# Kernel optimization log

Measured on AMD Instinct MI355X. Metric: run time of the kernel, lower is better.

## Reference

```python
import jax, jax.numpy as jnp
import numpy as np

SCALING = 32.0 / 16.0  # alpha / rank

def setup_inputs() -> dict:
    key = jax.random.key(0)
    k1, k2, k3, k4, k5 = jax.random.split(key, 5)
    B, S, D_IN, D_OUT, R = 4, 2048, 4096, 4096, 16
    x = jax.random.normal(k1, (B, S, D_IN), dtype=jnp.float32)
    weight_int = jax.random.randint(k2, (D_OUT, D_IN), -128, 128, dtype=jnp.int32)
    weight_scale = jax.random.uniform(k3, (1,), dtype=jnp.float32) * 0.01 + 1e-4
    lora_A = jax.random.normal(k4, (R, D_IN), dtype=jnp.float32) * (1.0 / np.sqrt(D_IN))
    lora_B = jax.random.normal(k5, (D_OUT, R), dtype=jnp.float32) * 0.02
    return {"x": x, "weight_int": weight_int, "weight_scale": weight_scale,
            "lora_A": lora_A, "lora_B": lora_B}

def reference(x, weight_int, weight_scale, lora_A, lora_B):
    # Dequantized base weight: [out, in]
    w = weight_int.astype(jnp.float32) * weight_scale  # broadcast scalar scale
    base = jnp.einsum('bsi,oi->bso', x, w)
    # Low-rank LoRA path: (x @ A^T) @ B^T * scaling
    lora = jnp.einsum('bsr,or->bso', jnp.einsum('bsi,ri->bsr', x, lora_A), lora_B) * SCALING
    return base + lora
```

## Files before the change

kernel.cpp:

```cpp
#include <hip/hip_runtime.h>

constexpr int M = 8192;
constexpr int N = 4096;
constexpr int K = 4096;
constexpr float SCALING = 2.0f;

typedef __bf16 bf16x8 __attribute__((ext_vector_type(8)));
typedef __bf16 bf16x4 __attribute__((ext_vector_type(4)));
typedef float  f32x4  __attribute__((ext_vector_type(4)));

__global__ __launch_bounds__(256) void qlora_cast_x(const float* __restrict__ x,
                                                    __bf16* __restrict__ xb) {
    const size_t i = ((size_t)blockIdx.x * 256 + threadIdx.x) * 8;
    const float4 v0 = *(const float4*)(x + i);
    const float4 v1 = *(const float4*)(x + i + 4);
    bf16x8 o;
    o[0] = (__bf16)v0.x; o[1] = (__bf16)v0.y; o[2] = (__bf16)v0.z; o[3] = (__bf16)v0.w;
    o[4] = (__bf16)v1.x; o[5] = (__bf16)v1.y; o[6] = (__bf16)v1.z; o[7] = (__bf16)v1.w;
    *(bf16x8*)(xb + i) = o;
}

__global__ __launch_bounds__(256) void qlora_prep_w(const int* __restrict__ wi,
                                                    const float* __restrict__ wscale,
                                                    const float* __restrict__ lA,
                                                    const float* __restrict__ lB,
                                                    __bf16* __restrict__ W) {
    __shared__ __align__(16) float As[16][1028];
    const int t  = threadIdx.x;
    const int ol = t >> 4;
    const int kk = t & 15;
    const int o  = blockIdx.x * 16 + ol;
    const float s = wscale[0];
    float b[16];
#pragma unroll
    for (int r = 0; r < 16; ++r) b[r] = lB[o * 16 + r];

    for (int c = 0; c < 4; ++c) {
        const int c0 = c * 1024;
#pragma unroll
        for (int i = 0; i < 16; ++i) {
            const int idx = t + i * 256;
            const int r   = idx >> 8;
            const int c4  = idx & 255;
            const float4 v = *(const float4*)(lA + r * K + c0 + c4 * 4);
            *(float4*)(&As[r][c4 * 4]) = v;
        }
        __syncthreads();
#pragma unroll
        for (int j = 0; j < 16; ++j) {
            const int k4 = kk + j * 16;
            const int kg = c0 + k4 * 4;
            const int4 w4 = *(const int4*)(wi + (size_t)o * K + kg);
            float a0 = 0.f, a1 = 0.f, a2 = 0.f, a3 = 0.f;
#pragma unroll
            for (int r = 0; r < 16; ++r) {
                const float4 a4 = *(const float4*)(&As[r][k4 * 4]);
                a0 += b[r] * a4.x; a1 += b[r] * a4.y;
                a2 += b[r] * a4.z; a3 += b[r] * a4.w;
            }
            bf16x4 v;
            v[0] = (__bf16)((float)w4.x * s + SCALING * a0);
            v[1] = (__bf16)((float)w4.y * s + SCALING * a1);
            v[2] = (__bf16)((float)w4.z * s + SCALING * a2);
            v[3] = (__bf16)((float)w4.w * s + SCALING * a3);
            *(bf16x4*)(W + (size_t)o * K + kg) = v;
        }
        __syncthreads();
    }
}

__device__ __forceinline__ void async16(const __bf16* g, __bf16* l) {
    __builtin_amdgcn_global_load_lds(
        (const __attribute__((address_space(1))) unsigned int*)(unsigned long long)g,
        (__attribute__((address_space(3))) unsigned int*)(unsigned int)(unsigned long long)l,
        16, 0, 0);
}

__global__ __launch_bounds__(512, 2) void qlora_gemm_bt(const __bf16* __restrict__ A,
                                                        const __bf16* __restrict__ B,
                                                        float* __restrict__ C) {
    __shared__ __align__(16) __bf16 Lds[65536];

    const int tid  = threadIdx.x;
    const int w    = tid >> 6;
    const int lane = tid & 63;
    const int quad = lane >> 4;
    const int lb   = lane & 15;
    const int wm   = w >> 2;
    const int wn   = w & 3;

    const int swz = (blockIdx.x & 7) * 64 + (blockIdx.x >> 3);
    const int bx  = swz >> 5;
    const int by  = swz & 31;
    const size_t mBase = (size_t)by * 256;
    const size_t nBase = (size_t)bx * 256;

    const int r16 = lane >> 2;
    const int ch  = ((lane & 3) ^ ((lane >> 3) & 3)) * 8;
    const __bf16* gA = A + (mBase + w * 32 + r16) * K + ch;
    const __bf16* gB = B + (nBase + w * 32 + r16) * K + ch;

    const int sw  = (quad ^ ((lb >> 1) & 3)) * 8;
    const int roA = (wm * 128 + lb) * 32 + sw;
    const int roB = (wn * 64 + lb) * 32 + sw;

    f32x4 acc[8][4] = {};

    auto stage = [&](int buf, int s) {
        __bf16* la  = Lds + buf * 16384 + w * 1024;
        __bf16* lbp = la + 8192;
        const __bf16* pa = gA + (size_t)s * 32;
        const __bf16* pb = gB + (size_t)s * 32;
        async16(pa, la);
        async16(pa + (size_t)16 * K, la + 512);
        async16(pb, lbp);
        async16(pb + (size_t)16 * K, lbp + 512);
    };

    auto MF = [](bf16x8 a, bf16x8 b, f32x4 c) {
        return __builtin_amdgcn_mfma_f32_16x16x32_bf16(a, b, c, 0, 0, 0);
    };

#define VM8 asm volatile("s_waitcnt vmcnt(8)" ::: "memory")
#define VM4 asm volatile("s_waitcnt vmcnt(4)" ::: "memory")
#define VM0 asm volatile("s_waitcnt vmcnt(0)" ::: "memory")
#define NOWAIT ((void)0)

#define GSTEP(BUF, DOSTAGE, SNEXT, WAITSTMT)                                 \
  {                                                                          \
    const __bf16* Ab = Lds + (BUF) * 16384;                                  \
    const __bf16* Bb = Ab + 8192;                                            \
    bf16x8 af[4], bfr[4];                                                    \
    _Pragma("unroll")                                                        \
    for (int fm = 0; fm < 4; ++fm)                                           \
      af[fm] = *(const bf16x8*)(Ab + roA + fm * 512);                        \
    _Pragma("unroll")                                                        \
    for (int fn = 0; fn < 4; ++fn)                                           \
      bfr[fn] = *(const bf16x8*)(Bb + roB + fn * 512);                       \
    if (DOSTAGE) stage((SNEXT) & 3, (SNEXT));                                \
    __builtin_amdgcn_s_barrier();                                            \
    asm volatile("s_waitcnt lgkmcnt(0)" ::: "memory");                       \
    __builtin_amdgcn_s_setprio(1);                                           \
    _Pragma("unroll")                                                        \
    for (int fm = 0; fm < 4; ++fm)                                           \
      _Pragma("unroll")                                                      \
      for (int fn = 0; fn < 4; ++fn)                                         \
        acc[fm][fn] = MF(af[fm], bfr[fn], acc[fm][fn]);                      \
    __builtin_amdgcn_s_setprio(0);                                           \
    __builtin_amdgcn_s_barrier();                                            \
    _Pragma("unroll")                                                        \
    for (int fm = 0; fm < 4; ++fm)                                           \
      af[fm] = *(const bf16x8*)(Ab + roA + (fm + 4) * 512);                  \
    __builtin_amdgcn_s_barrier();                                            \
    asm volatile("s_waitcnt lgkmcnt(0)" ::: "memory");                       \
    __builtin_amdgcn_s_setprio(1);                                           \
    _Pragma("unroll")                                                        \
    for (int fm = 0; fm < 4; ++fm)                                           \
      _Pragma("unroll")                                                      \
      for (int fn = 0; fn < 4; ++fn)                                         \
        acc[fm + 4][fn] = MF(af[fm], bfr[fn], acc[fm + 4][fn]);              \
    __builtin_amdgcn_s_setprio(0);                                           \
    WAITSTMT;                                                                \
    __builtin_amdgcn_s_barrier();                                            \
  }

    stage(0, 0);
    stage(1, 1);
    stage(2, 2);
    VM8;
    __builtin_amdgcn_s_barrier();

    for (int s = 0; s < 124; s += 4) {
        GSTEP(0, true, s + 3, VM8);
        GSTEP(1, true, s + 4, VM8);
        GSTEP(2, true, s + 5, VM8);
        GSTEP(3, true, s + 6, VM8);
    }
    GSTEP(0, true, 127, VM8);
    GSTEP(1, false, 0, VM4);
    GSTEP(2, false, 0, VM0);
    GSTEP(3, false, 0, NOWAIT);

#undef GSTEP
#undef VM8
#undef VM4
#undef VM0
#undef NOWAIT

#pragma unroll
    for (int fm = 0; fm < 8; ++fm) {
        const size_t m0 = mBase + wm * 128 + fm * 16 + quad * 4;
#pragma unroll
        for (int fn = 0; fn < 4; ++fn) {
            const size_t n0 = nBase + wn * 64 + fn * 16 + lb;
            float* p = C + m0 * N + n0;
            p[0 * (size_t)N] = acc[fm][fn][0];
            p[1 * (size_t)N] = acc[fm][fn][1];
            p[2 * (size_t)N] = acc[fm][fn][2];
            p[3 * (size_t)N] = acc[fm][fn][3];
        }
    }
}

extern "C" void kernel_launch(void* const* d_in, const int* in_sizes, int n_in,
                              void* d_out, int out_size, void* d_ws, size_t ws_size,
                              hipStream_t stream) {
    const float* x      = (const float*)d_in[0];
    const int*   wint   = (const int*)d_in[1];
    const float* wscale = (const float*)d_in[2];
    const float* lA     = (const float*)d_in[3];
    const float* lB     = (const float*)d_in[4];
    float* out = (float*)d_out;

    __bf16* Xb = (__bf16*)d_ws;
    __bf16* Wb = (__bf16*)((char*)d_ws + (size_t)M * K * 2);

    qlora_cast_x<<<16384, 256, 0, stream>>>(x, Xb);
    qlora_prep_w<<<256, 256, 0, stream>>>(wint, wscale, lA, lB, Wb);
    qlora_gemm_bt<<<dim3(512), dim3(512), 0, stream>>>(Xb, Wb, out);
}
```

Measured before the change: 545.8 us.

## Restructure GEMM pipeline to triple-buffered LDS with cross-step register prefetch

Cuts the LDS ring from four stages to three, freeing shared memory. Next-step A/B fragments now load from LDS interleaved with the current step's second MFMA half, so LDS reads overlap compute. Barriers per step drop from three to two. The trade-off is a shallower global prefetch distance and more live fragment registers, which may pressure occupancy at launch_bounds(512,2).

```diff
diff --git a/kernel.cpp b/kernel.cpp
--- a/kernel.cpp
+++ b/kernel.cpp
@@ -79,7 +79,7 @@
 __global__ __launch_bounds__(512, 2) void qlora_gemm_bt(const __bf16* __restrict__ A,
                                                         const __bf16* __restrict__ B,
                                                         float* __restrict__ C) {
-    __shared__ __align__(16) __bf16 Lds[65536];
+    __shared__ __align__(16) __bf16 Lds[49152];
 
     const int tid  = threadIdx.x;
     const int w    = tid >> 6;
@@ -105,9 +105,10 @@
     const int roB = (wn * 64 + lb) * 32 + sw;
 
     f32x4 acc[8][4] = {};
-
-    auto stage = [&](int buf, int s) {
-        __bf16* la  = Lds + buf * 16384 + w * 1024;
+    bf16x8 afL[4], afH[4], bfr[4];
+
+    auto stage = [&](int bufe, int s) {
+        __bf16* la  = Lds + bufe + w * 1024;
         __bf16* lbp = la + 8192;
         const __bf16* pa = gA + (size_t)s * 32;
         const __bf16* pb = gB + (size_t)s * 32;
@@ -121,71 +122,68 @@
         return __builtin_amdgcn_mfma_f32_16x16x32_bf16(a, b, c, 0, 0, 0);
     };
 
-#define VM8 asm volatile("s_waitcnt vmcnt(8)" ::: "memory")
-#define VM4 asm volatile("s_waitcnt vmcnt(4)" ::: "memory")
-#define VM0 asm volatile("s_waitcnt vmcnt(0)" ::: "memory")
-#define NOWAIT ((void)0)
-
-#define GSTEP(BUF, DOSTAGE, SNEXT, WAITSTMT)                                 \
+#define VM4  asm volatile("s_waitcnt vmcnt(4)" ::: "memory")
+#define VM0  asm volatile("s_waitcnt vmcnt(0)" ::: "memory")
+#define NOVM ((void)0)
+
+#define STEP(BC, BN, B2, DOSTAGE, MIDWAIT, DOPREF)                           \
   {                                                                          \
-    const __bf16* Ab = Lds + (BUF) * 16384;                                  \
-    const __bf16* Bb = Ab + 8192;                                            \
-    bf16x8 af[4], bfr[4];                                                    \
     _Pragma("unroll")                                                        \
-    for (int fm = 0; fm < 4; ++fm)                                           \
-      af[fm] = *(const bf16x8*)(Ab + roA + fm * 512);                        \
-    _Pragma("unroll")                                                        \
-    for (int fn = 0; fn < 4; ++fn)                                           \
-      bfr[fn] = *(const bf16x8*)(Bb + roB + fn * 512);                       \
-    if (DOSTAGE) stage((SNEXT) & 3, (SNEXT));                                \
-    __builtin_amdgcn_s_barrier();                                            \
-    asm volatile("s_waitcnt lgkmcnt(0)" ::: "memory");                       \
+    for (int f = 0; f < 4; ++f)                                              \
+      afH[f] = *(const bf16x8*)(Lds + (BC) + roA + (f + 4) * 512);           \
+    if (DOSTAGE) stage((B2), sStage);                                        \
+    asm volatile("s_waitcnt lgkmcnt(4)" ::: "memory");                       \
     __builtin_amdgcn_s_setprio(1);                                           \
     _Pragma("unroll")                                                        \
     for (int fm = 0; fm < 4; ++fm)                                           \
       _Pragma("unroll")                                                      \
       for (int fn = 0; fn < 4; ++fn)                                         \
-        acc[fm][fn] = MF(af[fm], bfr[fn], acc[fm][fn]);                      \
+        acc[fm][fn] = MF(afL[fm], bfr[fn], acc[fm][fn]);                     \
     __builtin_amdgcn_s_setprio(0);                                           \
-    __builtin_amdgcn_s_barrier();                                            \
-    _Pragma("unroll")                                                        \
-    for (int fm = 0; fm < 4; ++fm)                                           \
-      af[fm] = *(const bf16x8*)(Ab + roA + (fm + 4) * 512);                  \
+    MIDWAIT;                                                                 \
     __builtin_amdgcn_s_barrier();                                            \
     asm volatile("s_waitcnt lgkmcnt(0)" ::: "memory");                       \
     __builtin_amdgcn_s_setprio(1);                                           \
     _Pragma("unroll")                                                        \
-    for (int fm = 0; fm < 4; ++fm)                                           \
+    for (int fn = 0; fn < 4; ++fn) {                                         \
       _Pragma("unroll")                                                      \
-      for (int fn = 0; fn < 4; ++fn)                                         \
-        acc[fm + 4][fn] = MF(af[fm], bfr[fn], acc[fm + 4][fn]);              \
+      for (int fm = 0; fm < 4; ++fm)                                         \
+        acc[fm + 4][fn] = MF(afH[fm], bfr[fn], acc[fm + 4][fn]);             \
+      if (DOPREF) {                                                          \
+        bfr[fn] = *(const bf16x8*)(Lds + (BN) + 8192 + roB + fn * 512);      \
+        afL[fn] = *(const bf16x8*)(Lds + (BN) + roA + fn * 512);             \
+      }                                                                      \
+    }                                                                        \
     __builtin_amdgcn_s_setprio(0);                                           \
-    WAITSTMT;                                                                \
+    asm volatile("" ::: "memory");                                           \
     __builtin_amdgcn_s_barrier();                                            \
+    ++sStage;                                                                \
   }
 
+    int sStage = 2;
     stage(0, 0);
-    stage(1, 1);
-    stage(2, 2);
-    VM8;
+    stage(16384, 1);
+    VM4;
     __builtin_amdgcn_s_barrier();
-
-    for (int s = 0; s < 124; s += 4) {
-        GSTEP(0, true, s + 3, VM8);
-        GSTEP(1, true, s + 4, VM8);
-        GSTEP(2, true, s + 5, VM8);
-        GSTEP(3, true, s + 6, VM8);
-    }
-    GSTEP(0, true, 127, VM8);
-    GSTEP(1, false, 0, VM4);
-    GSTEP(2, false, 0, VM0);
-    GSTEP(3, false, 0, NOWAIT);
-
-#undef GSTEP
-#undef VM8
+#pragma unroll
+    for (int f = 0; f < 4; ++f) {
+        afL[f] = *(const bf16x8*)(Lds + roA + f * 512);
+        bfr[f] = *(const bf16x8*)(Lds + 8192 + roB + f * 512);
+    }
+    asm volatile("" ::: "memory");
+
+    for (int it = 0; it < 42; ++it) {
+        STEP(0,     16384, 32768, true, VM4, true);
+        STEP(16384, 32768, 0,     true, VM4, true);
+        STEP(32768, 0,     16384, true, VM4, true);
+    }
+    STEP(0,     16384, 32768, false, VM0,  true);
+    STEP(16384, 32768, 0,     false, NOVM, false);
+
+#undef STEP
 #undef VM4
 #undef VM0
-#undef NOWAIT
+#undef NOVM
 
 #pragma unroll
     for (int fm = 0; fm < 8; ++fm) {
```

Result: faster. 513.5 us (-5.9%).
